# Performance work log

Hardware: AMD Instinct MI355X
Metric: run time of the kernel (lower is better)

The kernel has to match this reference:

```python
import jax, jax.numpy as jnp
import numpy as np

B = 2048


def _maxpool2(x):
    return jax.lax.reduce_window(x, -jnp.inf, jax.lax.max,
                                 (1, 1, 2, 2), (1, 1, 2, 2), 'VALID')


def setup_inputs() -> dict:
    key = jax.random.key(0)
    ks = jax.random.split(key, 7)
    return {
        'x': jax.random.normal(ks[0], (B, 3, 32, 32), dtype=jnp.float32),
        'conv_w': jax.random.normal(ks[1], (45, 1, 5, 5), dtype=jnp.float32),
        'conv_b': jax.random.normal(ks[2], (45,), dtype=jnp.float32) * 0.1,
        'tree_w': jax.random.normal(ks[3], (1, 16, 15, 3, 7, 7, 2, 2), dtype=jnp.float32),
        'tree_b': jax.random.normal(ks[4], (1, 16, 3, 7), dtype=jnp.float32),
        'fc_w': jax.random.normal(ks[5], (10, 336), dtype=jnp.float32),
        'fc_b': jax.random.normal(ks[6], (10,), dtype=jnp.float32) * 0.1,
    }


def reference(x, conv_w, conv_b, tree_w, tree_b, fc_w, fc_b):
    # grouped conv: in=3, groups=3, out=45, kernel 5x5, VALID -> (B,45,28,28)
    out = jax.lax.conv_general_dilated(
        x, conv_w, window_strides=(1, 1), padding='VALID',
        dimension_numbers=('NCHW', 'OIHW', 'NCHW'), feature_group_count=3)
    out = jax.nn.sigmoid(out + conv_b[None, :, None, None])
    out = _maxpool2(out)  # (B,45,14,14)
    b = out.shape[0]
    # unfold((2,2),stride=2) + the torch reshape/transpose chain is equivalent to:
    # (B,45,14,14) -> (b, g=3, m=15, i=7, ki=2, j=7, kj=2) -> (b,m,g,i,j,ki,kj)
    xt = out.reshape(b, 3, 15, 7, 2, 7, 2).transpose(0, 2, 1, 3, 5, 4, 6)
    # TreeLayer: elementwise mul with weights (16,m,g,i,j,ki,kj) then sum over m,j,ki,kj
    t = jnp.einsum('bmgijkl,fmgijkl->bfgi', xt, tree_w[0]) + tree_b  # (B,16,3,7)
    t = jax.nn.sigmoid(t)
    return t.reshape(b, 16 * 3 * 7) @ fc_w.T + fc_b  # (B,10)
```

## Files before the change

kernel.cpp:

```cpp
#include <hip/hip_runtime.h>
#include <hip/hip_fp16.h>

#define BATCH 2048

typedef _Float16 f16x8 __attribute__((ext_vector_type(8)));
typedef float f32x4 __attribute__((ext_vector_type(4)));

#define RST 36
#define CST 1168
#define PIS 3152

__device__ __forceinline__ float fast_sigmoid(float v) {
    return __builtin_amdgcn_rcpf(1.0f + __builtin_amdgcn_exp2f(v * -1.44269504f));
}

#define WS_W3B  0
#define WS_FCW  301056

__global__ __launch_bounds__(256) void k_prep(
    const float* __restrict__ tree_w,
    const float* __restrict__ fc_w,
    ushort* __restrict__ W3B,
    float* __restrict__ FCW2,
    float* __restrict__ out)
{
    int pidx = blockIdx.x * 256 + threadIdx.x;
    if (pidx < 35280) {
        float4 v = ((const float4*)tree_w)[pidx];
        int j  = pidx % 7;
        int t1 = pidx / 7;
        int i  = t1 % 7;
        int t2 = t1 / 7;
        int g  = t2 % 3;
        int t3 = t2 / 3;
        int nn = t3 % 15;
        int f  = t3 / 15;
        int gi = g * 7 + i;
        int u  = nn & 7;
        int hi = nn >> 3;
        float vv[4] = {v.x, v.y, v.z, v.w};
        #pragma unroll
        for (int e = 0; e < 4; e++) {
            int ki = e >> 1, kj = e & 1;
            int u27 = ki * 14 + j * 2 + kj;
            int c   = u27 >> 1;
            int qq  = (u27 & 1) * 2 + hi;
            W3B[(size_t)(gi * 14 + c) * 512 + (qq * 16 + f) * 8 + u] =
                __half_as_ushort(__float2half(vv[e]));
        }
    } else if (pidx < 38640) {
        int jj = pidx - 35280;
        int f = jj & 15;
        int r = jj >> 4;
        int i = r % 7;
        int r2 = r / 7;
        int o = r2 % 10;
        int g = r2 / 10;
        FCW2[jj] = fc_w[o * 336 + f * 21 + g * 7 + i];
    } else if (pidx < 48048) {
        int z = pidx - 38640;
        int f  = z & 15;
        int qq = ((z >> 4) & 1) * 2 + 1;
        int r  = z >> 5;
        int c  = r % 14;
        int gi = r / 14;
        W3B[(size_t)(gi * 14 + c) * 512 + (qq * 16 + f) * 8 + 7] = 0;
    } else if (pidx < 68528) {
        out[pidx - 48048] = 0.f;
    }
}

__global__ __launch_bounds__(256, 4) void kF_all(
    const float* __restrict__ x,
    const float* __restrict__ conv_w,
    const float* __restrict__ conv_b,
    const ushort* __restrict__ W3B,
    const float* __restrict__ FCW2,
    const float* __restrict__ tree_b,
    const float* __restrict__ fc_b,
    float* __restrict__ out)
{
    __shared__ __align__(16) ushort xsc[4 * CST];
    __shared__ __align__(16) ushort ps[4 * PIS];
    ushort* tsl = xsc;

    const int tid  = threadIdx.x;
    const int blk  = blockIdx.x;
    const int quad = blk / 3;
    const int g    = blk - quad * 3;
    const int img0 = quad * 4;
    const int lane = tid & 63;
    const int n    = lane & 15;
    const int q    = lane >> 4;
    const int wave = tid >> 6;

    float4 xv[4];
    #pragma unroll
    for (int im = 0; im < 4; im++)
        xv[im] = ((const float4*)(x + (size_t)(img0 + im) * 3072 + g * 1024))[tid];

    f16x8 B1 = {0, 0, 0, 0, 0, 0, 0, 0};
    f16x8 B2 = {0, 0, 0, 0, 0, 0, 0, 0};
    float bs = 0.f;
    if (n < 15) {
        const float* wrow = conv_w + (g * 15 + n) * 25;
        #pragma unroll
        for (int u = 0; u < 5; u++) B1[u] = (_Float16)wrow[q * 5 + u];
        if (q == 0) {
            #pragma unroll
            for (int u = 0; u < 5; u++) B2[u] = (_Float16)wrow[20 + u];
        }
        bs = conv_b[g * 15 + n] * -1.44269504f;
    }

    const int dr = (n >> 1) & 1, dc = n & 1, n4 = n >> 2;
    const int a2c = (4 - q) * RST;
    int aoff[13];
    {
        int pb = wave * 4 + n4;
        int ph = (pb >= 14) ? 1 : 0;
        int pw = pb - 14 * ph;
        const int rbase = (dr + q) * RST;
        #pragma unroll
        for (int it = 0; it < 13; it++) {
            int s = 2 * (pw & 1) + dc;
            aoff[it] = s * CST + rbase + 2 * ph * RST + 4 * (pw >> 1);
            pw += 2; ph += 1;
            if (pw >= 14) { pw -= 14; ph += 1; }
        }
    }

    const int prow = tid >> 3, pt = tid & 7;
    ushort* const pbase = xsc + prow * RST + pt * 4;
    auto pack_img = [&](float4 v) {
        __half2 a = __float22half2_rn(make_float2(v.x, v.y));
        __half2 b = __float22half2_rn(make_float2(v.z, v.w));
        unsigned d0 = *(unsigned*)&a, d1 = *(unsigned*)&b;
        unsigned n0 = (unsigned)__shfl_down((int)d0, 1);
        unsigned n1 = (unsigned)__shfl_down((int)d1, 1);
        if (pt == 7) { n0 = 0u; n1 = 0u; }
        unsigned t01 = (d0 >> 16) | (d1 << 16);
        unsigned t12 = (d1 >> 16) | (n0 << 16);
        unsigned t23 = (n0 >> 16) | (n1 << 16);
        *(uint2*)(pbase)           = make_uint2(d0, d1);
        *(uint2*)(pbase + CST)     = make_uint2(t01, t12);
        *(uint2*)(pbase + 2 * CST) = make_uint2(d1, n0);
        *(uint2*)(pbase + 3 * CST) = make_uint2(t12, t23);
    };

    auto conv_tile = [&](int it, ushort* pso) {
        const ushort* pA = xsc + aoff[it];
        union U { struct { uint2 a, b; } u; f16x8 v; };
        U A1, A2;
        A1.u.a = *(const uint2*)pA;
        A1.u.b = *(const uint2*)(pA + 4);
        A2.u.a = *(const uint2*)(pA + a2c);
        A2.u.b = *(const uint2*)(pA + a2c + 4);
        f32x4 d = {0.f, 0.f, 0.f, 0.f};
        d = __builtin_amdgcn_mfma_f32_16x16x32_f16(A1.v, B1, d, 0, 0, 0);
        d = __builtin_amdgcn_mfma_f32_16x16x32_f16(A2.v, B2, d, 0, 0, 0);
        float mx = fmaxf(fmaxf(d[0], d[1]), fmaxf(d[2], d[3]));
        float e = __builtin_amdgcn_exp2f(fmaf(mx, -1.44269504f, bs));
        pso[(wave + it * 4) * 64 + lane] =
            __half_as_ushort(__float2half(__builtin_amdgcn_rcpf(1.0f + e)));
    };

    f16x8 Bf[14];

    #pragma unroll
    for (int rr = 0; rr < 4; rr++) {
        pack_img(xv[rr]);
        __syncthreads();
        if (rr == 3) {
            const f16x8* Wb = (const f16x8*)W3B + (size_t)(g * 7 + wave) * 896;
            #pragma unroll
            for (int c = 0; c < 14; c++) Bf[c] = Wb[c * 64 + lane];
        }
        ushort* pso = ps + rr * PIS;
        #pragma unroll
        for (int it = 0; it < 12; it++) conv_tile(it, pso);
        if (wave == 0) conv_tile(12, pso);
        __syncthreads();
    }

    auto tree_gemm = [&](int ii) {
        const ushort* ap = ps + (n & 3) * PIS + ii * 448;
        f32x4 D0 = {0.f, 0.f, 0.f, 0.f};
        f32x4 D1 = {0.f, 0.f, 0.f, 0.f};
        #pragma unroll
        for (int c = 0; c < 7; c++) {
            f16x8 Ae = *(const f16x8*)(ap + (2 * c) * 32 + q * 8);
            D0 = __builtin_amdgcn_mfma_f32_16x16x32_f16(Ae, Bf[2 * c], D0, 0, 0, 0);
            f16x8 Ao = *(const f16x8*)(ap + (2 * c + 1) * 32 + q * 8);
            D1 = __builtin_amdgcn_mfma_f32_16x16x32_f16(Ao, Bf[2 * c + 1], D1, 0, 0, 0);
        }
        if (q == 0) {
            float tb = tree_b[n * 21 + g * 7 + ii];
            #pragma unroll
            for (int im = 0; im < 4; im++) {
                float t = (D0[im] + D1[im]) + tb;
                tsl[(im * 7 + ii) * 16 + n] =
                    __half_as_ushort(__float2half(fast_sigmoid(t)));
            }
        }
    };

    tree_gemm(wave);
    if (wave < 3) {
        const f16x8* Wb = (const f16x8*)W3B + (size_t)(g * 7 + wave + 4) * 896;
        #pragma unroll
        for (int c = 0; c < 14; c++) Bf[c] = Wb[c * 64 + lane];
        tree_gemm(wave + 4);
    }
    __syncthreads();

    if (lane < 10) {
        const int im4 = wave, o = lane;
        const uint2* tp = (const uint2*)(tsl + im4 * 112);
        const float4* wp = (const float4*)(FCW2 + (size_t)(g * 10 + o) * 112);
        float acc = (g == 0) ? fc_b[o] : 0.f;
        #pragma unroll
        for (int jj = 0; jj < 28; jj++) {
            float4 w4 = wp[jj];
            uint2 hv = tp[jj];
            float2 p0 = __half22float2(*(const __half2*)&hv.x);
            float2 p1 = __half22float2(*(const __half2*)&hv.y);
            acc = fmaf(p0.x, w4.x, acc);
            acc = fmaf(p0.y, w4.y, acc);
            acc = fmaf(p1.x, w4.z, acc);
            acc = fmaf(p1.y, w4.w, acc);
        }
#if defined(__HIP_PLATFORM_AMD__)
        unsafeAtomicAdd(out + (size_t)(img0 + im4) * 10 + o, acc);
#else
        atomicAdd(out + (size_t)(img0 + im4) * 10 + o, acc);
#endif
    }
}

extern "C" void kernel_launch(void* const* d_in, const int* in_sizes, int n_in,
                              void* d_out, int out_size, void* d_ws, size_t ws_size,
                              hipStream_t stream) {
    const float* x      = (const float*)d_in[0];
    const float* conv_w = (const float*)d_in[1];
    const float* conv_b = (const float*)d_in[2];
    const float* tree_w = (const float*)d_in[3];
    const float* tree_b = (const float*)d_in[4];
    const float* fc_w   = (const float*)d_in[5];
    const float* fc_b   = (const float*)d_in[6];
    float* out = (float*)d_out;

    ushort* W3B  = (ushort*)((char*)d_ws + WS_W3B);
    float*  FCW2 = (float*)((char*)d_ws + WS_FCW);

    k_prep<<<268, 256, 0, stream>>>(tree_w, fc_w, W3B, FCW2, out);
    kF_all<<<512 * 3, 256, 0, stream>>>(x, conv_w, conv_b, W3B, FCW2,
                                        tree_b, fc_b, out);
}
```

Before: 109.5 us.

## Halve conv staging LDS with dword-shifted planes and raise occupancy

The fp16 image staging buffer now stores two column-shift planes at dword granularity instead of four halfword-shift planes. This cuts the LDS footprint and the pack stores. The conv A operands are gathered with dword reads at arbitrary column offsets. The tree-GEMM weight prefetch is moved out of the conv loop into a simple per-row loop, which lowers register pressure, and the launch bound is raised to 5 blocks per CU. The trade-off is that the early weight-load overlap is lost and A-fragment loads become narrower.

```diff
diff --git a/kernel.cpp b/kernel.cpp
--- a/kernel.cpp
+++ b/kernel.cpp
@@ -6,9 +6,9 @@
 typedef _Float16 f16x8 __attribute__((ext_vector_type(8)));
 typedef float f32x4 __attribute__((ext_vector_type(4)));
 
-#define RST 36
-#define CST 1168
-#define PIS 3152
+#define XROW 18
+#define XPL  584
+#define PIS  3152
 
 __device__ __forceinline__ float fast_sigmoid(float v) {
     return __builtin_amdgcn_rcpf(1.0f + __builtin_amdgcn_exp2f(v * -1.44269504f));
@@ -70,7 +70,7 @@
     }
 }
 
-__global__ __launch_bounds__(256, 4) void kF_all(
+__global__ __launch_bounds__(256, 5) void kF_all(
     const float* __restrict__ x,
     const float* __restrict__ conv_w,
     const float* __restrict__ conv_b,
@@ -80,9 +80,9 @@
     const float* __restrict__ fc_b,
     float* __restrict__ out)
 {
-    __shared__ __align__(16) ushort xsc[4 * CST];
+    __shared__ __align__(16) unsigned xsc[2 * XPL];
     __shared__ __align__(16) ushort ps[4 * PIS];
-    ushort* tsl = xsc;
+    ushort* tsl = (ushort*)xsc;
 
     const int tid  = threadIdx.x;
     const int blk  = blockIdx.x;
@@ -99,6 +99,11 @@
     for (int im = 0; im < 4; im++)
         xv[im] = ((const float4*)(x + (size_t)(img0 + im) * 3072 + g * 1024))[tid];
 
+    if (tid < 64) {
+        int pl = tid >> 5, row = tid & 31;
+        *(uint2*)&xsc[pl * XPL + row * XROW + 16] = make_uint2(0u, 0u);
+    }
+
     f16x8 B1 = {0, 0, 0, 0, 0, 0, 0, 0};
     f16x8 B2 = {0, 0, 0, 0, 0, 0, 0, 0};
     float bs = 0.f;
@@ -114,48 +119,44 @@
     }
 
     const int dr = (n >> 1) & 1, dc = n & 1, n4 = n >> 2;
-    const int a2c = (4 - q) * RST;
-    int aoff[13];
+    const int a2cd = (4 - q) * XROW;
+    int aoffd[13];
     {
         int pb = wave * 4 + n4;
         int ph = (pb >= 14) ? 1 : 0;
         int pw = pb - 14 * ph;
-        const int rbase = (dr + q) * RST;
+        int base = dc * XPL + (dr + q) * XROW;
         #pragma unroll
         for (int it = 0; it < 13; it++) {
-            int s = 2 * (pw & 1) + dc;
-            aoff[it] = s * CST + rbase + 2 * ph * RST + 4 * (pw >> 1);
+            aoffd[it] = base + 2 * ph * XROW + pw;
             pw += 2; ph += 1;
             if (pw >= 14) { pw -= 14; ph += 1; }
         }
     }
 
     const int prow = tid >> 3, pt = tid & 7;
-    ushort* const pbase = xsc + prow * RST + pt * 4;
+    unsigned* const pbase = xsc + prow * XROW + 2 * pt;
     auto pack_img = [&](float4 v) {
         __half2 a = __float22half2_rn(make_float2(v.x, v.y));
         __half2 b = __float22half2_rn(make_float2(v.z, v.w));
         unsigned d0 = *(unsigned*)&a, d1 = *(unsigned*)&b;
         unsigned n0 = (unsigned)__shfl_down((int)d0, 1);
-        unsigned n1 = (unsigned)__shfl_down((int)d1, 1);
-        if (pt == 7) { n0 = 0u; n1 = 0u; }
+        if (pt == 7) n0 = 0u;
         unsigned t01 = (d0 >> 16) | (d1 << 16);
         unsigned t12 = (d1 >> 16) | (n0 << 16);
-        unsigned t23 = (n0 >> 16) | (n1 << 16);
-        *(uint2*)(pbase)           = make_uint2(d0, d1);
-        *(uint2*)(pbase + CST)     = make_uint2(t01, t12);
-        *(uint2*)(pbase + 2 * CST) = make_uint2(d1, n0);
-        *(uint2*)(pbase + 3 * CST) = make_uint2(t12, t23);
+        *(uint2*)(pbase)       = make_uint2(d0, d1);
+        *(uint2*)(pbase + XPL) = make_uint2(t01, t12);
     };
 
     auto conv_tile = [&](int it, ushort* pso) {
-        const ushort* pA = xsc + aoff[it];
-        union U { struct { uint2 a, b; } u; f16x8 v; };
+        const unsigned* p0 = xsc + aoffd[it];
+        union U { unsigned w[4]; f16x8 v; };
         U A1, A2;
-        A1.u.a = *(const uint2*)pA;
-        A1.u.b = *(const uint2*)(pA + 4);
-        A2.u.a = *(const uint2*)(pA + a2c);
-        A2.u.b = *(const uint2*)(pA + a2c + 4);
+        #pragma unroll
+        for (int e = 0; e < 4; e++) {
+            A1.w[e] = p0[e];
+            A2.w[e] = p0[a2cd + e];
+        }
         f32x4 d = {0.f, 0.f, 0.f, 0.f};
         d = __builtin_amdgcn_mfma_f32_16x16x32_f16(A1.v, B1, d, 0, 0, 0);
         d = __builtin_amdgcn_mfma_f32_16x16x32_f16(A2.v, B2, d, 0, 0, 0);
@@ -165,17 +166,10 @@
             __half_as_ushort(__float2half(__builtin_amdgcn_rcpf(1.0f + e)));
     };
 
-    f16x8 Bf[14];
-
     #pragma unroll
     for (int rr = 0; rr < 4; rr++) {
         pack_img(xv[rr]);
         __syncthreads();
-        if (rr == 3) {
-            const f16x8* Wb = (const f16x8*)W3B + (size_t)(g * 7 + wave) * 896;
-            #pragma unroll
-            for (int c = 0; c < 14; c++) Bf[c] = Wb[c * 64 + lane];
-        }
         ushort* pso = ps + rr * PIS;
         #pragma unroll
         for (int it = 0; it < 12; it++) conv_tile(it, pso);
@@ -183,8 +177,12 @@
         __syncthreads();
     }
 
-    auto tree_gemm = [&](int ii) {
+    for (int ii = wave; ii < 7; ii += 4) {
+        const f16x8* Wb = (const f16x8*)W3B + (size_t)(g * 7 + ii) * 896;
         const ushort* ap = ps + (n & 3) * PIS + ii * 448;
+        f16x8 Bf[14];
+        #pragma unroll
+        for (int c = 0; c < 14; c++) Bf[c] = Wb[c * 64 + lane];
         f32x4 D0 = {0.f, 0.f, 0.f, 0.f};
         f32x4 D1 = {0.f, 0.f, 0.f, 0.f};
         #pragma unroll
@@ -203,14 +201,6 @@
                     __half_as_ushort(__float2half(fast_sigmoid(t)));
             }
         }
-    };
-
-    tree_gemm(wave);
-    if (wave < 3) {
-        const f16x8* Wb = (const f16x8*)W3B + (size_t)(g * 7 + wave + 4) * 896;
-        #pragma unroll
-        for (int c = 0; c < 14; c++) Bf[c] = Wb[c * 64 + lane];
-        tree_gemm(wave + 4);
     }
     __syncthreads();
 
```

After: 102.5 us (median of 2 runs). 6.5% less time.
